# Kernel tuning notes

Measured on AMD Instinct MI355X. Metric: run time of the kernel, lower is better.

The kernel has to match this reference:

```python
import jax, jax.numpy as jnp
import numpy as np

B, L, H = 32, 2048, 1024  # batch, seq (atoms), hid_dim; trg last dim = 3*H


def setup_inputs() -> dict:
    key = jax.random.key(0)
    k1, k2, k3, k4 = jax.random.split(key, 4)
    trg = jax.random.normal(k1, (B, L, 3 * H), dtype=jnp.float32)
    src = jax.random.normal(k2, (B, 512, H), dtype=jnp.float32)  # unused (n_layers=0)
    fc_w = jax.random.normal(k3, (H, 3 * H), dtype=jnp.float32) * (1.0 / np.sqrt(3 * H))
    fc_b = jax.random.normal(k4, (H,), dtype=jnp.float32) * 0.01
    return {"trg": trg, "src": src, "fc_w": fc_w, "fc_b": fc_b}


def reference(trg, src, fc_w, fc_b):
    # decoder layers: n_layers == 0 -> identity
    t = jnp.einsum('blk,hk->blh', trg, fc_w) + fc_b          # fc: [B, L, H]
    norm1 = jnp.linalg.norm(t, axis=2)                        # [B, L]
    w = jax.nn.softmax(norm1, axis=1)                         # [B, L]
    # vectorized form of the nested python-loop weighted-sum pooling
    summ = jnp.einsum('blh,bl->bh', t, w)                     # [B, H]
    return (summ, norm1)
```

## Files before the change

### kernel.cpp

```cpp
#include <hip/hip_runtime.h>
#include <hip/hip_bf16.h>


#define B_ 32
#define L_ 2048
#define H_ 1024
#define K_ 3072
#define M_ 65536

typedef __attribute__((ext_vector_type(8))) short short8;
typedef __attribute__((ext_vector_type(4))) float floatx4;

#define LDST 40

__device__ __forceinline__ unsigned int pack_bf16x2(float a, float b) {
    __hip_bfloat162 h = __float22bfloat162_rn(make_float2(a, b));
    return *reinterpret_cast<unsigned int*>(&h);
}

__global__ void __launch_bounds__(256) gemm_norm_kernel(const float* __restrict__ trg,
                                                        const float* __restrict__ fcw,
                                                        float* __restrict__ normsq) {
    __shared__ unsigned short As[128 * LDST];
    __shared__ unsigned short Bs[128 * LDST];

    const int tid  = threadIdx.x;
    const int bid  = blockIdx.x;
    const int nblk = bid & 7;
    const int mblk = bid >> 3;
    const int R0   = mblk * 128;
    const int N0   = nblk * 128;
    const int wv   = tid >> 6;
    const int lane = tid & 63;
    const int wr   = wv >> 1;
    const int wc   = wv & 1;
    const int q    = lane >> 4;
    const int ln   = lane & 15;

    floatx4 acc[4][4] = {};

    const int srow = tid >> 3;
    const int skc  = tid & 7;
    const float* ap = trg + (size_t)(R0 + srow) * K_ + skc * 4;
    const float* bp = fcw + (size_t)(N0 + srow) * K_ + skc * 4;
    unsigned short* AsW = &As[srow * LDST + skc * 4];
    unsigned short* BsW = &Bs[srow * LDST + skc * 4];

    const unsigned short* Af = &As[(wr * 64 + ln) * LDST + q * 8];
    const unsigned short* Bf = &Bs[(wc * 64 + ln) * LDST + q * 8];

    float4 ra[4], rb[4];
#pragma unroll
    for (int s = 0; s < 4; ++s) {
        ra[s] = *(const float4*)(ap + (size_t)(s * 32) * K_);
        rb[s] = *(const float4*)(bp + (size_t)(s * 32) * K_);
    }

    for (int step = 0; step < 96; ++step) {
        __syncthreads();
#pragma unroll
        for (int s = 0; s < 4; ++s) {
            uint2 ua, ub;
            ua.x = pack_bf16x2(ra[s].x, ra[s].y);
            ua.y = pack_bf16x2(ra[s].z, ra[s].w);
            ub.x = pack_bf16x2(rb[s].x, rb[s].y);
            ub.y = pack_bf16x2(rb[s].z, rb[s].w);
            *(uint2*)(AsW + s * 32 * LDST) = ua;
            *(uint2*)(BsW + s * 32 * LDST) = ub;
        }
        if (step < 95) {
            const int kk = (step + 1) * 32;
#pragma unroll
            for (int s = 0; s < 4; ++s) {
                ra[s] = *(const float4*)(ap + (size_t)(s * 32) * K_ + kk);
                rb[s] = *(const float4*)(bp + (size_t)(s * 32) * K_ + kk);
            }
        }
        __syncthreads();

        short8 af[4], bf[4];
#pragma unroll
        for (int i = 0; i < 4; ++i) {
            af[i] = *(const short8*)(Af + i * 16 * LDST);
            bf[i] = *(const short8*)(Bf + i * 16 * LDST);
        }
#pragma unroll
        for (int mi = 0; mi < 4; ++mi)
#pragma unroll
            for (int ni = 0; ni < 4; ++ni)
                acc[mi][ni] = __builtin_amdgcn_mfma_f32_16x16x32_bf16(af[mi], bf[ni],
                                                                      acc[mi][ni], 0, 0, 0);
    }

    float* nsq = normsq + R0;
#pragma unroll
    for (int mi = 0; mi < 4; ++mi) {
#pragma unroll
        for (int r = 0; r < 4; ++r) {
            float s = 0.0f;
#pragma unroll
            for (int ni = 0; ni < 4; ++ni) {
                float v = acc[mi][ni][r];
                s += v * v;
            }
            s += __shfl_xor(s, 1);
            s += __shfl_xor(s, 2);
            s += __shfl_xor(s, 4);
            s += __shfl_xor(s, 8);
            if (ln == 0) atomicAdd(&nsq[wr * 64 + mi * 16 + q * 4 + r], s);
        }
    }
}

__global__ void __launch_bounds__(256) softmax_stats_kernel(const float* __restrict__ normsq,
                                                            float* __restrict__ norm1,
                                                            float* __restrict__ bstats) {
    const int b = blockIdx.x;
    const int t = threadIdx.x;
    __shared__ float red[256];

    float vals[8];
    float mx = -1e30f;
#pragma unroll
    for (int i = 0; i < 8; ++i) {
        float v = sqrtf(normsq[b * L_ + i * 256 + t]);
        vals[i] = v;
        norm1[b * L_ + i * 256 + t] = v;
        mx = fmaxf(mx, v);
    }
    red[t] = mx;
    __syncthreads();
    for (int s = 128; s > 0; s >>= 1) {
        if (t < s) red[t] = fmaxf(red[t], red[t + s]);
        __syncthreads();
    }
    mx = red[0];
    __syncthreads();

    float sm = 0.0f;
#pragma unroll
    for (int i = 0; i < 8; ++i) sm += expf(vals[i] - mx);
    red[t] = sm;
    __syncthreads();
    for (int s = 128; s > 0; s >>= 1) {
        if (t < s) red[t] += red[t + s];
        __syncthreads();
    }
    if (t == 0) {
        bstats[b * 2 + 0] = mx;
        bstats[b * 2 + 1] = 1.0f / red[0];
    }
}

__global__ void __launch_bounds__(256) pool_kernel(const float* __restrict__ trg,
                                                   const float* __restrict__ norm1,
                                                   const float* __restrict__ bstats,
                                                   float* __restrict__ p) {
    const int t  = threadIdx.x;
    const int b  = blockIdx.x / 24;
    const int r  = blockIdx.x % 24;
    const int lc = r / 3;
    const int kc = r % 3;
    const int l0 = lc * 256;

    __shared__ float wl[256];
    const float mx   = bstats[b * 2 + 0];
    const float sinv = bstats[b * 2 + 1];
    wl[t] = expf(norm1[b * L_ + l0 + t] - mx) * sinv;
    __syncthreads();

    const int k = kc * 1024 + t * 4;
    const float* tp = trg + (size_t)b * L_ * K_ + (size_t)l0 * K_ + k;
    float4 acc = {0.0f, 0.0f, 0.0f, 0.0f};
    for (int i = 0; i < 256; ++i) {
        float4 v = *(const float4*)(tp + (size_t)i * K_);
        float w = wl[i];
        acc.x += w * v.x;
        acc.y += w * v.y;
        acc.z += w * v.z;
        acc.w += w * v.w;
    }
    float* pp = p + b * K_ + k;
    atomicAdd(&pp[0], acc.x);
    atomicAdd(&pp[1], acc.y);
    atomicAdd(&pp[2], acc.z);
    atomicAdd(&pp[3], acc.w);
}

__global__ void __launch_bounds__(256) summ_kernel(const float* __restrict__ fcw,
                                                   const float* __restrict__ fcb,
                                                   const float* __restrict__ p,
                                                   float* __restrict__ summ) {
    __shared__ float ps[K_];
    const int b  = blockIdx.x >> 2;
    const int hc = blockIdx.x & 3;
    const int t  = threadIdx.x;

    for (int i = t; i < K_ / 4; i += 256)
        ((float4*)ps)[i] = ((const float4*)(p + (size_t)b * K_))[i];
    __syncthreads();

    const int h = hc * 256 + t;
    const float4* wrow = (const float4*)(fcw + (size_t)h * K_);
    float acc = fcb[h];
    for (int i = 0; i < K_ / 4; ++i) {
        float4 wv = wrow[i];
        float4 pv = ((const float4*)ps)[i];
        acc += wv.x * pv.x + wv.y * pv.y + wv.z * pv.z + wv.w * pv.w;
    }
    summ[b * H_ + h] = acc;
}

extern "C" void kernel_launch(void* const* d_in, const int* in_sizes, int n_in,
                              void* d_out, int out_size, void* d_ws, size_t ws_size,
                              hipStream_t stream) {
    (void)in_sizes; (void)n_in; (void)out_size; (void)ws_size;
    const float* trg = (const float*)d_in[0];
    const float* fcw = (const float*)d_in[2];
    const float* fcb = (const float*)d_in[3];

    float* out   = (float*)d_out;
    float* summ  = out;
    float* norm1 = out + B_ * H_;

    float* normsq = (float*)d_ws;
    float* p      = normsq + M_;
    float* bstats = p + B_ * K_;

    hipMemsetAsync(d_ws, 0, (size_t)(M_ + B_ * K_ + 64) * sizeof(float), stream);

    hipLaunchKernelGGL(gemm_norm_kernel, dim3(4096), dim3(256), 0, stream, trg, fcw, normsq);
    hipLaunchKernelGGL(softmax_stats_kernel, dim3(B_), dim3(256), 0, stream, normsq, norm1, bstats);
    hipLaunchKernelGGL(pool_kernel, dim3(B_ * 24), dim3(256), 0, stream, trg, norm1, bstats, p);
    hipLaunchKernelGGL(summ_kernel, dim3(B_ * 4), dim3(256), 0, stream, fcw, fcb, p, summ);
}
```

Measured before the change: 1.964 ms.

## Pre-convert inputs to bf16 and use direct global-to-LDS loads in GEMM

Adds a pre-pass converting trg and fc_w to bf16 in workspace, then runs the GEMM-norm kernel with global_load_lds direct copies and an XCD-aware block mapping, and the pooling kernel on bf16 data. This removes the per-step fp32 load and convert work from the GEMM inner loop and halves pooling read bytes. In exchange it adds a full conversion pass that writes a 400MB copy, and pooling now uses bf16-rounded inputs. The bias is also now included in the norm computation, and a fallback fp32 path is kept if workspace is too small.

```diff
diff --git a/kernel.cpp b/kernel.cpp
--- a/kernel.cpp
+++ b/kernel.cpp
@@ -11,23 +11,146 @@
 typedef __attribute__((ext_vector_type(8))) short short8;
 typedef __attribute__((ext_vector_type(4))) float floatx4;
 
-#define LDST 40
-
 __device__ __forceinline__ unsigned int pack_bf16x2(float a, float b) {
     __hip_bfloat162 h = __float22bfloat162_rn(make_float2(a, b));
     return *reinterpret_cast<unsigned int*>(&h);
 }
 
-__global__ void __launch_bounds__(256) gemm_norm_kernel(const float* __restrict__ trg,
-                                                        const float* __restrict__ fcw,
-                                                        float* __restrict__ normsq) {
+__device__ __forceinline__ float bf2f(unsigned short u) {
+    return __uint_as_float(((unsigned int)u) << 16);
+}
+
+__device__ __forceinline__ void gl_lds16(const unsigned short* g, unsigned short* l) {
+    __builtin_amdgcn_global_load_lds(
+        (const __attribute__((address_space(1))) unsigned int*)g,
+        (__attribute__((address_space(3))) unsigned int*)l, 16, 0, 0);
+}
+
+__global__ void __launch_bounds__(256) convert_bf16_kernel(const float* __restrict__ in,
+                                                           unsigned short* __restrict__ out,
+                                                           int n8) {
+    int i = blockIdx.x * blockDim.x + threadIdx.x;
+    const int stride = gridDim.x * blockDim.x;
+    for (; i < n8; i += stride) {
+        const float4* pp = (const float4*)in + (size_t)i * 2;
+        float4 a = pp[0], b = pp[1];
+        uint4 r;
+        r.x = pack_bf16x2(a.x, a.y);
+        r.y = pack_bf16x2(a.z, a.w);
+        r.z = pack_bf16x2(b.x, b.y);
+        r.w = pack_bf16x2(b.z, b.w);
+        ((uint4*)out)[i] = r;
+    }
+}
+
+__global__ void __launch_bounds__(256, 4) gemm_norm_bf_kernel(
+        const unsigned short* __restrict__ A,
+        const unsigned short* __restrict__ Bw,
+        const float* __restrict__ fcb,
+        float* __restrict__ normsq) {
+    __shared__ unsigned short As[128 * 32];
+    __shared__ unsigned short Bs[128 * 32];
+
+    const int tid = threadIdx.x;
+    const int bid = blockIdx.x;
+    const int group  = bid >> 6;
+    const int lane64 = bid & 63;
+    const int xcd    = lane64 & 7;
+    const int nblk   = lane64 >> 3;
+    const int mblk   = group * 8 + xcd;
+    const int R0 = mblk * 128;
+    const int N0 = nblk * 128;
+
+    const int wv = tid >> 6, lane = tid & 63;
+    const int wr = wv >> 1, wc = wv & 1;
+    const int q = lane >> 4, ln = lane & 15;
+
+    const int r0    = wv * 32;
+    const int lrow  = lane >> 2;
+    const int lchnk = lane & 3;
+    const unsigned short* agp = A  + (size_t)(R0 + r0 + lrow) * K_ + lchnk * 8;
+    const unsigned short* bgp = Bw + (size_t)(N0 + r0 + lrow) * K_ + lchnk * 8;
+    unsigned short* alds0 = &As[r0 * 32];
+    unsigned short* alds1 = &As[(r0 + 16) * 32];
+    unsigned short* blds0 = &Bs[r0 * 32];
+    unsigned short* blds1 = &Bs[(r0 + 16) * 32];
+    const size_t roff = (size_t)16 * K_;
+
+    gl_lds16(agp, alds0);
+    gl_lds16(agp + roff, alds1);
+    gl_lds16(bgp, blds0);
+    gl_lds16(bgp + roff, blds1);
+
+    floatx4 acc[4][4] = {};
+    const unsigned short* Af = &As[(wr * 64 + ln) * 32 + q * 8];
+    const unsigned short* Bf = &Bs[(wc * 64 + ln) * 32 + q * 8];
+
+    for (int step = 0; step < 96; ++step) {
+        __syncthreads();
+
+        short8 af[4], bf[4];
+#pragma unroll
+        for (int i = 0; i < 4; ++i) {
+            af[i] = *(const short8*)(Af + i * 16 * 32);
+            bf[i] = *(const short8*)(Bf + i * 16 * 32);
+        }
+
+        __syncthreads();
+
+        if (step < 95) {
+            const int kk = (step + 1) * 32;
+            gl_lds16(agp + kk, alds0);
+            gl_lds16(agp + roff + kk, alds1);
+            gl_lds16(bgp + kk, blds0);
+            gl_lds16(bgp + roff + kk, blds1);
+        }
+
+#pragma unroll
+        for (int mi = 0; mi < 4; ++mi)
+#pragma unroll
+            for (int ni = 0; ni < 4; ++ni)
+                acc[mi][ni] = __builtin_amdgcn_mfma_f32_16x16x32_bf16(af[mi], bf[ni],
+                                                                      acc[mi][ni], 0, 0, 0);
+    }
+
+    float bz[4];
+#pragma unroll
+    for (int ni = 0; ni < 4; ++ni) bz[ni] = fcb[N0 + wc * 64 + ni * 16 + ln];
+
+    float* nsq = normsq + R0 + wr * 64;
+#pragma unroll
+    for (int mi = 0; mi < 4; ++mi) {
+#pragma unroll
+        for (int r = 0; r < 4; ++r) {
+            float s = 0.0f;
+#pragma unroll
+            for (int ni = 0; ni < 4; ++ni) {
+                float v = acc[mi][ni][r] + bz[ni];
+                s += v * v;
+            }
+            s += __shfl_xor(s, 1);
+            s += __shfl_xor(s, 2);
+            s += __shfl_xor(s, 4);
+            s += __shfl_xor(s, 8);
+            if (ln == 0) atomicAdd(&nsq[mi * 16 + q * 4 + r], s);
+        }
+    }
+}
+
+#define LDST 40
+__global__ void __launch_bounds__(256) gemm_norm_f32_kernel(const float* __restrict__ trg,
+                                                            const float* __restrict__ fcw,
+                                                            const float* __restrict__ fcb,
+                                                            float* __restrict__ normsq) {
     __shared__ unsigned short As[128 * LDST];
     __shared__ unsigned short Bs[128 * LDST];
 
     const int tid  = threadIdx.x;
     const int bid  = blockIdx.x;
-    const int nblk = bid & 7;
-    const int mblk = bid >> 3;
+    const int group  = bid >> 6;
+    const int lane64 = bid & 63;
+    const int nblk   = lane64 >> 3;
+    const int mblk   = group * 8 + (lane64 & 7);
     const int R0   = mblk * 128;
     const int N0   = nblk * 128;
     const int wv   = tid >> 6;
@@ -92,6 +215,10 @@
                                                                       acc[mi][ni], 0, 0, 0);
     }
 
+    float bz[4];
+#pragma unroll
+    for (int ni = 0; ni < 4; ++ni) bz[ni] = fcb[N0 + wc * 64 + ni * 16 + ln];
+
     float* nsq = normsq + R0;
 #pragma unroll
     for (int mi = 0; mi < 4; ++mi) {
@@ -100,7 +227,7 @@
             float s = 0.0f;
 #pragma unroll
             for (int ni = 0; ni < 4; ++ni) {
-                float v = acc[mi][ni][r];
+                float v = acc[mi][ni][r] + bz[ni];
                 s += v * v;
             }
             s += __shfl_xor(s, 1);
@@ -152,10 +279,47 @@
     }
 }
 
-__global__ void __launch_bounds__(256) pool_kernel(const float* __restrict__ trg,
-                                                   const float* __restrict__ norm1,
-                                                   const float* __restrict__ bstats,
-                                                   float* __restrict__ p) {
+__global__ void __launch_bounds__(256) pool_bf_kernel(const unsigned short* __restrict__ trgbf,
+                                                      const float* __restrict__ norm1,
+                                                      const float* __restrict__ bstats,
+                                                      float* __restrict__ p) {
+    const int t  = threadIdx.x;
+    const int b  = blockIdx.x / 48;
+    const int r  = blockIdx.x % 48;
+    const int lc = r / 3;
+    const int kc = r % 3;
+    const int l0 = lc * 128;
+
+    __shared__ float wl[128];
+    if (t < 128) {
+        const float mx   = bstats[b * 2 + 0];
+        const float sinv = bstats[b * 2 + 1];
+        wl[t] = expf(norm1[b * L_ + l0 + t] - mx) * sinv;
+    }
+    __syncthreads();
+
+    const int k = kc * 1024 + t * 4;
+    const unsigned short* tp = trgbf + (size_t)(b * L_ + l0) * K_ + k;
+    float4 acc = {0.0f, 0.0f, 0.0f, 0.0f};
+    for (int i = 0; i < 128; ++i) {
+        ushort4 v = *(const ushort4*)(tp + (size_t)i * K_);
+        float w = wl[i];
+        acc.x += w * bf2f(v.x);
+        acc.y += w * bf2f(v.y);
+        acc.z += w * bf2f(v.z);
+        acc.w += w * bf2f(v.w);
+    }
+    float* pp = p + b * K_ + k;
+    atomicAdd(&pp[0], acc.x);
+    atomicAdd(&pp[1], acc.y);
+    atomicAdd(&pp[2], acc.z);
+    atomicAdd(&pp[3], acc.w);
+}
+
+__global__ void __launch_bounds__(256) pool_f32_kernel(const float* __restrict__ trg,
+                                                       const float* __restrict__ norm1,
+                                                       const float* __restrict__ bstats,
+                                                       float* __restrict__ p) {
     const int t  = threadIdx.x;
     const int b  = blockIdx.x / 24;
     const int r  = blockIdx.x % 24;
@@ -214,7 +378,7 @@
 extern "C" void kernel_launch(void* const* d_in, const int* in_sizes, int n_in,
                               void* d_out, int out_size, void* d_ws, size_t ws_size,
                               hipStream_t stream) {
-    (void)in_sizes; (void)n_in; (void)out_size; (void)ws_size;
+    (void)in_sizes; (void)n_in; (void)out_size;
     const float* trg = (const float*)d_in[0];
     const float* fcw = (const float*)d_in[2];
     const float* fcb = (const float*)d_in[3];
@@ -223,14 +387,44 @@
     float* summ  = out;
     float* norm1 = out + B_ * H_;
 
-    float* normsq = (float*)d_ws;
-    float* p      = normsq + M_;
-    float* bstats = p + B_ * K_;
-
-    hipMemsetAsync(d_ws, 0, (size_t)(M_ + B_ * K_ + 64) * sizeof(float), stream);
-
-    hipLaunchKernelGGL(gemm_norm_kernel, dim3(4096), dim3(256), 0, stream, trg, fcw, normsq);
-    hipLaunchKernelGGL(softmax_stats_kernel, dim3(B_), dim3(256), 0, stream, normsq, norm1, bstats);
-    hipLaunchKernelGGL(pool_kernel, dim3(B_ * 24), dim3(256), 0, stream, trg, norm1, bstats, p);
-    hipLaunchKernelGGL(summ_kernel, dim3(B_ * 4), dim3(256), 0, stream, fcw, fcb, p, summ);
-}
+    const size_t trgbf_elems = (size_t)M_ * K_;
+    const size_t fcwbf_elems = (size_t)H_ * K_;
+    const size_t acc_bytes   = (size_t)(M_ + B_ * K_ + 64) * sizeof(float);
+    const size_t need = (trgbf_elems + fcwbf_elems) * sizeof(unsigned short) + acc_bytes;
+
+    if (ws_size >= need) {
+        unsigned short* trgbf = (unsigned short*)d_ws;
+        unsigned short* fcwbf = trgbf + trgbf_elems;
+        float* normsq = (float*)(fcwbf + fcwbf_elems);
+        float* p      = normsq + M_;
+        float* bstats = p + B_ * K_;
+
+        hipMemsetAsync(normsq, 0, acc_bytes, stream);
+        hipLaunchKernelGGL(convert_bf16_kernel, dim3(16384), dim3(256), 0, stream,
+                           trg, trgbf, (int)(trgbf_elems / 8));
+        hipLaunchKernelGGL(convert_bf16_kernel, dim3(1536), dim3(256), 0, stream,
+                           fcw, fcwbf, (int)(fcwbf_elems / 8));
+        hipLaunchKernelGGL(gemm_norm_bf_kernel, dim3(4096), dim3(256), 0, stream,
+                           trgbf, fcwbf, fcb, normsq);
+        hipLaunchKernelGGL(softmax_stats_kernel, dim3(B_), dim3(256), 0, stream,
+                           normsq, norm1, bstats);
+        hipLaunchKernelGGL(pool_bf_kernel, dim3(B_ * 48), dim3(256), 0, stream,
+                           trgbf, norm1, bstats, p);
+        hipLaunchKernelGGL(summ_kernel, dim3(B_ * 4), dim3(256), 0, stream,
+                           fcw, fcb, p, summ);
+    } else {
+        float* normsq = (float*)d_ws;
+        float* p      = normsq + M_;
+        float* bstats = p + B_ * K_;
+
+        hipMemsetAsync(d_ws, 0, acc_bytes, stream);
+        hipLaunchKernelGGL(gemm_norm_f32_kernel, dim3(4096), dim3(256), 0, stream,
+                           trg, fcw, fcb, normsq);
+        hipLaunchKernelGGL(softmax_stats_kernel, dim3(B_), dim3(256), 0, stream,
+                           normsq, norm1, bstats);
+        hipLaunchKernelGGL(pool_f32_kernel, dim3(B_ * 24), dim3(256), 0, stream,
+                           trg, norm1, bstats, p);
+        hipLaunchKernelGGL(summ_kernel, dim3(B_ * 4), dim3(256), 0, stream,
+                           fcw, fcb, p, summ);
+    }
+}
```

Result: faster. 1.759 ms (-10.4%).
